# Performance work log

Measured on AMD Instinct MI355X. Metric: run time of the kernel, lower is better.

## Reference

```python
import jax, jax.numpy as jnp
import numpy as np
from jax import lax

N, DEG = 32768, 16

def _leaky(x):
    return jnp.where(x > 0, x, 0.2 * x)

def _gatv2(h, src, ws, bs, wd, bd, attn, bias):
    # DGL GATv2Conv: e_uv = attn . leaky_relu(fc_src(h_u) + fc_dst(h_v)); edge softmax over in-neighbors
    Hn, Dn = attn.shape
    fs = (h @ ws + bs).reshape(N, Hn, Dn)
    fd = (h @ wd + bd).reshape(N, Hn, Dn)
    e = _leaky(fs[src] + fd[:, None])                          # [N, DEG, H, D]
    alpha = jax.nn.softmax(jnp.einsum('ndhk,hk->ndh', e, attn), axis=1)
    return jnp.einsum('ndh,ndhk->nhk', alpha, fs[src]) + bias.reshape(1, Hn, Dn)

def _lstm_last(x, wih, whh, b):
    # torch LSTM gate order i,f,g,o; returns final hidden state. x: [N, DEG, F]
    n, hh = x.shape[0], whh.shape[1]
    def step(carry, xt):
        h, c = carry
        g = xt @ wih.T + h @ whh.T + b
        i, f, gg, o = jnp.split(g, 4, axis=-1)
        c = jax.nn.sigmoid(f) * c + jax.nn.sigmoid(i) * jnp.tanh(gg)
        h = jax.nn.sigmoid(o) * jnp.tanh(c)
        return (h, c), None
    init = (jnp.zeros((n, hh), x.dtype), jnp.zeros((n, hh), x.dtype))
    (h, _), _ = lax.scan(step, init, jnp.swapaxes(x, 0, 1))
    return h

def _sage(h, src, wih, whh, b, wself, wneigh, bias):
    # DGL SAGEConv(aggregator='lstm'): rst = fc_self(h) + fc_neigh(lstm(neighbor msgs))
    hn = _lstm_last(h[src], wih, whh, b)
    return h @ wself + hn @ wneigh + bias

def _forward(feat, g0, l0, g1, l1, g2, l2, s1, s2, f1_w, f1_b, f2_w, f2_b, src):
    h = feat
    h = jax.nn.elu(_gatv2(h, src, *g0).reshape(N, -1) + h @ l0[0] + l0[1])
    h = jax.nn.elu(_gatv2(h, src, *g1).reshape(N, -1) + h @ l1[0] + l1[1])
    gat = _gatv2(h, src, *g2).mean(axis=1) + h @ l2[0] + l2[1]   # [N, 32]
    x = jax.nn.relu(_sage(feat, src, *s1))
    x = jax.nn.relu(_sage(x, src, *s2))                          # [N, 32]
    z = jnp.concatenate([gat, x], axis=1)
    z = jax.nn.relu(z @ f1_w + f1_b)
    return z @ f2_w + f2_b                                       # [N, 1]

def setup_inputs() -> dict:
    ks = iter(jax.random.split(jax.random.key(0), 64))
    def nrm(shape, s=0.1):
        return (s * jax.random.normal(next(ks), shape)).astype(jnp.float32)
    d = {}
    d['feat'] = jax.random.normal(next(ks), (N, 5), jnp.float32)
    d['src'] = jax.random.randint(next(ks), (N, DEG), 0, N)
    for i, (fi, hn) in enumerate([(5, 4), (128, 4), (128, 1)]):
        fo = 32 * hn
        d[f'g{i}_ws'] = nrm((fi, fo)); d[f'g{i}_bs'] = nrm((fo,))
        d[f'g{i}_wd'] = nrm((fi, fo)); d[f'g{i}_bd'] = nrm((fo,))
        d[f'g{i}_attn'] = nrm((hn, 32)); d[f'g{i}_bias'] = nrm((fo,))
        d[f'l{i}_w'] = nrm((fi, fo)); d[f'l{i}_b'] = nrm((fo,))
    for j, fi in [(1, 5), (2, 32)]:
        d[f's{j}_wih'] = nrm((4 * fi, fi)); d[f's{j}_whh'] = nrm((4 * fi, fi))
        d[f's{j}_b'] = nrm((4 * fi,))
        d[f's{j}_wself'] = nrm((fi, 32)); d[f's{j}_wneigh'] = nrm((fi, 32))
        d[f's{j}_bias'] = nrm((32,))
    d['f1_w'] = nrm((64, 16)); d['f1_b'] = nrm((16,))
    d['f2_w'] = (0.1 + 0.01 * jax.random.normal(next(ks), (16, 1))).astype(jnp.float32)
    d['f2_b'] = nrm((1,))
    return d

def reference(feat, src, g0_ws, g0_bs, g0_wd, g0_bd, g0_attn, g0_bias, l0_w, l0_b, g1_ws, g1_bs, g1_wd, g1_bd, g1_attn, g1_bias, l1_w, l1_b, g2_ws, g2_bs, g2_wd, g2_bd, g2_attn, g2_bias, l2_w, l2_b, s1_wih, s1_whh, s1_b, s1_wself, s1_wneigh, s1_bias, s2_wih, s2_whh, s2_b, s2_wself, s2_wneigh, s2_bias, f1_w, f1_b, f2_w, f2_b):
    return _forward(feat,
                    (g0_ws, g0_bs, g0_wd, g0_bd, g0_attn, g0_bias), (l0_w, l0_b),
                    (g1_ws, g1_bs, g1_wd, g1_bd, g1_attn, g1_bias), (l1_w, l1_b),
                    (g2_ws, g2_bs, g2_wd, g2_bd, g2_attn, g2_bias), (l2_w, l2_b),
                    (s1_wih, s1_whh, s1_b, s1_wself, s1_wneigh, s1_bias),
                    (s2_wih, s2_whh, s2_b, s2_wself, s2_wneigh, s2_bias),
                    f1_w, f1_b, f2_w, f2_b, src)
```

## Files before the change

kernel.cpp:

```cpp
#include <hip/hip_runtime.h>
#include <hip/hip_bf16.h>

#define NNODES 32768
#define DEG 16

__device__ __forceinline__ float sigmoidf_(float x) { return 1.f / (1.f + __expf(-x)); }
__device__ __forceinline__ float tanhf_(float x) { return 1.f - 2.f / (__expf(2.f * x) + 1.f); }

typedef __attribute__((ext_vector_type(8))) short bf16x8;
typedef __attribute__((ext_vector_type(4))) float f32x4;
typedef __attribute__((ext_vector_type(8))) _Float16 f16x8;

__device__ __forceinline__ unsigned short f2bf_(float x) {
  __hip_bfloat16 b = __float2bfloat16(x);
  union { __hip_bfloat16 b; unsigned short u; } cv;
  cv.b = b;
  return cv.u;
}
__device__ __forceinline__ float bf2f_(unsigned short u) {
  union { unsigned short u; __hip_bfloat16 b; } cv;
  cv.u = u;
  return __bfloat162float(cv.b);
}
__device__ __forceinline__ void pack_hilo_(const float* v, bf16x8& hi, bf16x8& lo) {
#pragma unroll
  for (int j = 0; j < 8; j++) {
    unsigned short h = f2bf_(v[j]);
    float resid = v[j] - bf2f_(h);
    hi[j] = (short)h;
    lo[j] = (short)f2bf_(resid);
  }
}

#define WP_G1    0
#define WP_G2    98304
#define WP_S2WIH 122880
#define WP_TOTAL 131072

__global__ __launch_bounds__(256) void startup_kernel(
    const float* __restrict__ feat,
    const float* __restrict__ W0, const float* __restrict__ B0,
    const float* __restrict__ W1, const float* __restrict__ B1,
    const float* __restrict__ W2, const float* __restrict__ B2,
    float* __restrict__ O0, float* __restrict__ O1, float* __restrict__ O2,
    const float* __restrict__ g1ws, const float* __restrict__ g1wd,
    const float* __restrict__ l1w, const float* __restrict__ g2ws,
    const float* __restrict__ g2wd, const float* __restrict__ l2w,
    const float* __restrict__ s2wih, short* __restrict__ Wp) {
  __shared__ float w_s[5 * 64];
  __shared__ float in_s[32 * 8];
  __shared__ float b_s[64];
  const int bid = blockIdx.x;
  const int t = threadIdx.x;
  if (bid < 6144) {
    const int bz = bid >> 11, rem = bid & 2047, by = rem >> 10, bx = rem & 1023;
    const float* W = (bz == 0) ? W0 : (bz == 1) ? W1 : W2;
    const float* bias = (bz == 0) ? B0 : (bz == 1) ? B1 : B2;
    float* out = (bz == 0) ? O0 : (bz == 1) ? O1 : O2;
    const int rowBase = bx * 32;
    const int colBase = by * 64;
    for (int idx = t; idx < 5 * 64; idx += 256) {
      int k = idx >> 6, jj = idx & 63;
      w_s[idx] = W[(size_t)k * 128 + colBase + jj];
    }
    if (t < 64) b_s[t] = bias[colBase + t];
    for (int idx = t; idx < 32 * 5; idx += 256) {
      int r = idx / 5, k = idx - r * 5;
      in_s[r * 8 + k] = feat[(size_t)(rowBase + r) * 5 + k];
    }
    __syncthreads();
    const int jj = t & 63;
    const int rslot = t >> 6;
    float acc[8];
#pragma unroll
    for (int r = 0; r < 8; r++) acc[r] = b_s[jj];
    {
      float wv0 = w_s[0 * 64 + jj], wv1 = w_s[1 * 64 + jj];
      float wv2 = w_s[2 * 64 + jj], wv3 = w_s[3 * 64 + jj];
#pragma unroll
      for (int r = 0; r < 8; r++) {
        float4 ip = *(const float4*)&in_s[(rslot * 8 + r) * 8];
        acc[r] += ip.x * wv0 + ip.y * wv1 + ip.z * wv2 + ip.w * wv3;
      }
      float wv4 = w_s[4 * 64 + jj];
#pragma unroll
      for (int r = 0; r < 8; r++) acc[r] += in_s[(rslot * 8 + r) * 8 + 4] * wv4;
    }
#pragma unroll
    for (int r = 0; r < 8; r++)
      out[(size_t)(rowBase + rslot * 8 + r) * 128 + colBase + jj] = acc[r];
  } else {
    const int mid = bid - 6144;
    const float* W;
    int FI, FO, TRANS;
    size_t base;
    if (mid == 0)      { W = g1ws;  FI = 128; FO = 128; TRANS = 0; base = WP_G1; }
    else if (mid == 1) { W = g1wd;  FI = 128; FO = 128; TRANS = 0; base = WP_G1 + 32768; }
    else if (mid == 2) { W = l1w;   FI = 128; FO = 128; TRANS = 0; base = WP_G1 + 65536; }
    else if (mid == 3) { W = g2ws;  FI = 128; FO = 32;  TRANS = 0; base = WP_G2; }
    else if (mid == 4) { W = g2wd;  FI = 128; FO = 32;  TRANS = 0; base = WP_G2 + 8192; }
    else if (mid == 5) { W = l2w;   FI = 128; FO = 32;  TRANS = 0; base = WP_G2 + 16384; }
    else               { W = s2wih; FI = 32;  FO = 128; TRANS = 1; base = WP_S2WIH; }
    const int KS = FI / 32;
    const int total = FI * FO;
    for (int p = t; p < total; p += 256) {
      int j = p & 7, lane = (p >> 3) & 63, rest = p >> 9;
      int ks = rest % KS, f = rest / KS;
      int n = lane & 15, q = lane >> 4;
      int k = 32 * ks + 8 * q + j, fo = 16 * f + n;
      float v = TRANS ? W[(size_t)fo * FI + k] : W[(size_t)k * FO + fo];
      unsigned short hi = f2bf_(v);
      float resid = v - bf2f_(hi);
      Wp[base + p] = (short)hi;
      Wp[base + total + p] = (short)f2bf_(resid);
    }
  }
}

template <int KS, int FOT, int NZ>
__global__ __launch_bounds__(256) __attribute__((amdgpu_waves_per_eu(1, 4)))
void mfma_fc_kernel(const float* __restrict__ in, const short* __restrict__ Wp,
                    const float* __restrict__ B0, const float* __restrict__ B1,
                    const float* __restrict__ B2, float* __restrict__ O0,
                    float* __restrict__ O1, float* __restrict__ O2) {
  constexpr int FI = 32 * KS;
  constexpr int FO = 16 * FOT;
  const int tid = threadIdx.x;
  const int wid = tid >> 6;
  const int lane = tid & 63;
  const int q = lane >> 4, n = lane & 15;
  const int n0 = blockIdx.x * 64 + wid * 16;
  bf16x8 Ahi[KS], Alo[KS];
#pragma unroll
  for (int ks = 0; ks < KS; ks++) {
    float av[8];
    *(float4*)&av[0] = *(const float4*)&in[(size_t)(n0 + n) * FI + 32 * ks + 8 * q];
    *(float4*)&av[4] = *(const float4*)&in[(size_t)(n0 + n) * FI + 32 * ks + 8 * q + 4];
    pack_hilo_(av, Ahi[ks], Alo[ks]);
  }
#pragma unroll
  for (int z = 0; z < NZ; z++) {
    const short* wz = Wp + (size_t)z * FI * FO * 2;
    const float* bz = (z == 0) ? B0 : (z == 1) ? B1 : B2;
    float* oz = (z == 0) ? O0 : (z == 1) ? O1 : O2;
#pragma unroll
    for (int f = 0; f < FOT; f++) {
      float bv = bz[16 * f + n];
      f32x4 acc = {bv, bv, bv, bv};
#pragma unroll
      for (int ks = 0; ks < KS; ks++) {
        bf16x8 Bhi = *(const bf16x8*)&wz[((size_t)(f * KS + ks) * 64 + lane) * 8];
        bf16x8 Blo = *(const bf16x8*)&wz[(size_t)FI * FO + ((size_t)(f * KS + ks) * 64 + lane) * 8];
        acc = __builtin_amdgcn_mfma_f32_16x16x32_bf16(Ahi[ks], Bhi, acc, 0, 0, 0);
        acc = __builtin_amdgcn_mfma_f32_16x16x32_bf16(Alo[ks], Bhi, acc, 0, 0, 0);
        acc = __builtin_amdgcn_mfma_f32_16x16x32_bf16(Ahi[ks], Blo, acc, 0, 0, 0);
      }
#pragma unroll
      for (int r = 0; r < 4; r++)
        oz[(size_t)(n0 + 4 * q + r) * FO + 16 * f + n] = acc[r];
    }
  }
}

__global__ __launch_bounds__(256) __attribute__((amdgpu_waves_per_eu(1, 4)))
void xw_half_kernel(const float* __restrict__ in, const short* __restrict__ Wp,
                    const float* __restrict__ bz, _Float16* __restrict__ XWh) {
  const int tid = threadIdx.x;
  const int wid = tid >> 6;
  const int lane = tid & 63;
  const int q = lane >> 4, n = lane & 15;
  const int n0 = blockIdx.x * 64 + wid * 16;
  bf16x8 Ahi, Alo;
  {
    float av[8];
    *(float4*)&av[0] = *(const float4*)&in[(size_t)(n0 + n) * 32 + 8 * q];
    *(float4*)&av[4] = *(const float4*)&in[(size_t)(n0 + n) * 32 + 8 * q + 4];
    pack_hilo_(av, Ahi, Alo);
  }
#pragma unroll
  for (int f = 0; f < 8; f++) {
    float bv = bz[16 * f + n];
    f32x4 acc = {bv, bv, bv, bv};
    bf16x8 Bhi = *(const bf16x8*)&Wp[((size_t)f * 64 + lane) * 8];
    bf16x8 Blo = *(const bf16x8*)&Wp[4096 + ((size_t)f * 64 + lane) * 8];
    acc = __builtin_amdgcn_mfma_f32_16x16x32_bf16(Ahi, Bhi, acc, 0, 0, 0);
    acc = __builtin_amdgcn_mfma_f32_16x16x32_bf16(Alo, Bhi, acc, 0, 0, 0);
    acc = __builtin_amdgcn_mfma_f32_16x16x32_bf16(Ahi, Blo, acc, 0, 0, 0);
#pragma unroll
    for (int r = 0; r < 4; r++)
      XWh[(size_t)(n0 + 4 * q + r) * 128 + ((n >> 2) * 32 + f * 4 + (n & 3))] =
          (_Float16)acc[r];
  }
}

__global__ __launch_bounds__(256) void gat4_kernel(const float* __restrict__ fs,
                                                   const float* __restrict__ fd,
                                                   const float* __restrict__ lin,
                                                   const int* __restrict__ src,
                                                   const float* __restrict__ attn,
                                                   const float* __restrict__ bias,
                                                   float* __restrict__ out) {
  constexpr int F = 128;
  const int lane = threadIdx.x & 63;
  const int wave = threadIdx.x >> 6;
  const int li = lane & 15;
  const int node = blockIdx.x * 4 + wave;
  const int f0 = 2 * lane;
  const int srcv = src[(size_t)node * DEG + li];
  const float2 fdv = *(const float2*)&fd[(size_t)node * F + f0];
  const float a0 = attn[f0];
  const float a1 = attn[f0 + 1];
  float m = -1e30f, s = 0.f, acc0 = 0.f, acc1 = 0.f;
  int sd = __shfl(srcv, (lane & 48), 64);
  float2 fsv = *(const float2*)&fs[(size_t)sd * F + f0];
#pragma unroll
  for (int d = 0; d < DEG; d++) {
    float2 cur = fsv;
    if (d < DEG - 1) {
      int sn = __shfl(srcv, (lane & 48) | (d + 1), 64);
      fsv = *(const float2*)&fs[(size_t)sn * F + f0];
    }
    float e0 = cur.x + fdv.x; e0 = (e0 > 0.f) ? e0 : 0.2f * e0;
    float e1 = cur.y + fdv.y; e1 = (e1 > 0.f) ? e1 : 0.2f * e1;
    float p = e0 * a0 + e1 * a1;
    p += __shfl_xor(p, 1, 64);
    p += __shfl_xor(p, 2, 64);
    p += __shfl_xor(p, 4, 64);
    p += __shfl_xor(p, 8, 64);
    float nm = fmaxf(m, p);
    float ex = __expf(p - nm);
    float sc = __expf(m - nm);
    s = s * sc + ex;
    acc0 = acc0 * sc + ex * cur.x;
    acc1 = acc1 * sc + ex * cur.y;
    m = nm;
  }
  float inv = 1.f / s;
  float2 lv = *(const float2*)&lin[(size_t)node * F + f0];
  float o0 = acc0 * inv + lv.x + bias[f0];
  float o1 = acc1 * inv + lv.y + bias[f0 + 1];
  o0 = (o0 > 0.f) ? o0 : __expf(o0) - 1.f;
  o1 = (o1 > 0.f) ? o1 : __expf(o1) - 1.f;
  *(float2*)&out[(size_t)node * F + f0] = make_float2(o0, o1);
}

__global__ __launch_bounds__(256) void gat1_fw1_kernel(
    const float* __restrict__ fs, const float* __restrict__ fd,
    const float* __restrict__ lin, const int* __restrict__ src,
    const float* __restrict__ attn, const float* __restrict__ bias,
    float* __restrict__ out, const float* __restrict__ feat,
    const float* __restrict__ wih, const float* __restrict__ wb,
    float* __restrict__ fwout) {
  __shared__ float w_s[100];
  __shared__ float b_s[20];
  if (blockIdx.x < 2048) {
    constexpr int F = 32;
    const int lane = threadIdx.x & 63;
    const int wave = threadIdx.x >> 6;
    const int G = lane >> 4, li = lane & 15;
    const int node = blockIdx.x * 16 + wave * 4 + G;
    const int f0 = 2 * li;
    const int srcv = src[(size_t)node * DEG + li];
    const float2 fdv = *(const float2*)&fd[(size_t)node * F + f0];
    const float a0 = attn[f0];
    const float a1 = attn[f0 + 1];
    float m = -1e30f, s = 0.f, acc0 = 0.f, acc1 = 0.f;
    int sd = __shfl(srcv, (lane & 48), 64);
    float2 fsv = *(const float2*)&fs[(size_t)sd * F + f0];
#pragma unroll
    for (int d = 0; d < DEG; d++) {
      float2 cur = fsv;
      if (d < DEG - 1) {
        int sn = __shfl(srcv, (lane & 48) | (d + 1), 64);
        fsv = *(const float2*)&fs[(size_t)sn * F + f0];
      }
      float e0 = cur.x + fdv.x; e0 = (e0 > 0.f) ? e0 : 0.2f * e0;
      float e1 = cur.y + fdv.y; e1 = (e1 > 0.f) ? e1 : 0.2f * e1;
      float p = e0 * a0 + e1 * a1;
      p += __shfl_xor(p, 1, 64);
      p += __shfl_xor(p, 2, 64);
      p += __shfl_xor(p, 4, 64);
      p += __shfl_xor(p, 8, 64);
      float nm = fmaxf(m, p);
      float ex = __expf(p - nm);
      float sc = __expf(m - nm);
      s = s * sc + ex;
      acc0 = acc0 * sc + ex * cur.x;
      acc1 = acc1 * sc + ex * cur.y;
      m = nm;
    }
    float inv = 1.f / s;
    float2 lv = *(const float2*)&lin[(size_t)node * F + f0];
    float o0 = acc0 * inv + lv.x + bias[f0];
    float o1 = acc1 * inv + lv.y + bias[f0 + 1];
    *(float2*)&out[(size_t)node * F + f0] = make_float2(o0, o1);
  } else {
    if (threadIdx.x < 100) w_s[threadIdx.x] = wih[threadIdx.x];
    if (threadIdx.x < 20) b_s[threadIdx.x] = wb[threadIdx.x];
    __syncthreads();
    const int n = (blockIdx.x - 2048) * 256 + threadIdx.x;
    float f[5];
#pragma unroll
    for (int k = 0; k < 5; k++) f[k] = feat[(size_t)n * 5 + k];
#pragma unroll
    for (int j = 0; j < 20; j++) {
      float a = b_s[j];
#pragma unroll
      for (int k = 0; k < 5; k++) a += f[k] * w_s[j * 5 + k];
      fwout[(size_t)n * 20 + j] = a;
    }
  }
}

__global__ __attribute__((amdgpu_waves_per_eu(1, 4))) __launch_bounds__(256)
void lstm1s_kernel(const float* __restrict__ FW, const int* __restrict__ src,
                   const float* __restrict__ whh, const float* __restrict__ feat,
                   const float* __restrict__ wself, const float* __restrict__ wneigh,
                   const float* __restrict__ bias, float* __restrict__ x1out) {
  __shared__ float w_s[100];
  __shared__ float ws_s[160];
  __shared__ float wn_s[160];
  __shared__ float b_s[32];
  if (threadIdx.x < 100) w_s[threadIdx.x] = whh[threadIdx.x];
  if (threadIdx.x < 160) {
    ws_s[threadIdx.x] = wself[threadIdx.x];
    wn_s[threadIdx.x] = wneigh[threadIdx.x];
  }
  if (threadIdx.x < 32) b_s[threadIdx.x] = bias[threadIdx.x];
  __syncthreads();
  const int n = blockIdx.x * 256 + threadIdx.x;
  const int* sp = src + (size_t)n * DEG;
  float f[5];
#pragma unroll
  for (int k = 0; k < 5; k++) f[k] = feat[(size_t)n * 5 + k];
  float h[5] = {0, 0, 0, 0, 0}, c[5] = {0, 0, 0, 0, 0};
  int sd = sp[0];
  float4 p0 = *(const float4*)&FW[(size_t)sd * 20 + 0];
  float4 p1 = *(const float4*)&FW[(size_t)sd * 20 + 4];
  float4 p2 = *(const float4*)&FW[(size_t)sd * 20 + 8];
  float4 p3 = *(const float4*)&FW[(size_t)sd * 20 + 12];
  float4 p4 = *(const float4*)&FW[(size_t)sd * 20 + 16];
  for (int d = 0; d < DEG; d++) {
    float g[20];
    g[0] = p0.x; g[1] = p0.y; g[2] = p0.z; g[3] = p0.w;
    g[4] = p1.x; g[5] = p1.y; g[6] = p1.z; g[7] = p1.w;
    g[8] = p2.x; g[9] = p2.y; g[10] = p2.z; g[11] = p2.w;
    g[12] = p3.x; g[13] = p3.y; g[14] = p3.z; g[15] = p3.w;
    g[16] = p4.x; g[17] = p4.y; g[18] = p4.z; g[19] = p4.w;
    if (d < DEG - 1) {
      int sn = sp[d + 1];
      p0 = *(const float4*)&FW[(size_t)sn * 20 + 0];
      p1 = *(const float4*)&FW[(size_t)sn * 20 + 4];
      p2 = *(const float4*)&FW[(size_t)sn * 20 + 8];
      p3 = *(const float4*)&FW[(size_t)sn * 20 + 12];
      p4 = *(const float4*)&FW[(size_t)sn * 20 + 16];
    }
#pragma unroll
    for (int j = 0; j < 20; j++) {
#pragma unroll
      for (int k = 0; k < 5; k++) g[j] += h[k] * w_s[j * 5 + k];
    }
#pragma unroll
    for (int k = 0; k < 5; k++) {
      float iv = sigmoidf_(g[k]);
      float fv = sigmoidf_(g[5 + k]);
      float gv = tanhf_(g[10 + k]);
      float ov = sigmoidf_(g[15 + k]);
      c[k] = fv * c[k] + iv * gv;
      h[k] = ov * tanhf_(c[k]);
    }
  }
#pragma unroll
  for (int j = 0; j < 32; j++) {
    float a = b_s[j];
#pragma unroll
    for (int k = 0; k < 5; k++) a += f[k] * ws_s[k * 32 + j] + h[k] * wn_s[k * 32 + j];
    x1out[(size_t)n * 32 + j] = fmaxf(a, 0.f);
  }
}

__global__ __launch_bounds__(256) __attribute__((amdgpu_waves_per_eu(1, 4)))
void lstm2_mfma_kernel(const _Float16* __restrict__ XW, const int* __restrict__ src,
                       const float* __restrict__ whh, float* __restrict__ hn_out) {
  __shared__ float h_lds_all[4 * 16 * 36];
  __shared__ int src_lds_all[4 * 256];
  const int tid = threadIdx.x;
  const int wid = tid >> 6;
  const int lane = tid & 63;
  const int q = lane >> 4;
  const int n = lane & 15;
  const int n0 = (blockIdx.x * 4 + wid) * 16;
  float* h_lds = &h_lds_all[wid * 16 * 36];
  int* src_lds = &src_lds_all[wid * 256];

  {
    int4 sv = *(const int4*)&src[(size_t)(n0 + (lane >> 2)) * DEG + 4 * (lane & 3)];
    src_lds[(4 * (lane & 3) + 0) * 16 + (lane >> 2)] = sv.x;
    src_lds[(4 * (lane & 3) + 1) * 16 + (lane >> 2)] = sv.y;
    src_lds[(4 * (lane & 3) + 2) * 16 + (lane >> 2)] = sv.z;
    src_lds[(4 * (lane & 3) + 3) * 16 + (lane >> 2)] = sv.w;
  }

  bf16x8 Whi[8], Wlo[8];
#pragma unroll
  for (int gt = 0; gt < 8; gt++) {
    float wv[8];
    *(float4*)&wv[0] = *(const float4*)&whh[(size_t)(16 * gt + n) * 32 + 8 * q];
    *(float4*)&wv[4] = *(const float4*)&whh[(size_t)(16 * gt + n) * 32 + 8 * q + 4];
    pack_hilo_(wv, Whi[gt], Wlo[gt]);
  }

  bf16x8 Bhi, Blo;
#pragma unroll
  for (int j = 0; j < 8; j++) { Bhi[j] = 0; Blo[j] = 0; }
  float cst[8];
#pragma unroll
  for (int i = 0; i < 8; i++) cst[i] = 0.f;

  f16x8 tch[4], tnh[4];
  {
    int s0 = src_lds[0 * 16 + n];
    const _Float16* gb = XW + (size_t)s0 * 128 + q * 32;
#pragma unroll
    for (int t = 0; t < 4; t++) tch[t] = *(const f16x8*)&gb[8 * t];
  }

  float hv[8];
#pragma unroll
  for (int d = 0; d < DEG; d++) {
    f32x4 D[4][2];
#pragma unroll
    for (int p = 0; p < 4; p++) {
#pragma unroll
      for (int hh = 0; hh < 2; hh++) {
        int gt = p * 2 + hh;
        f32x4 acc = {0.f, 0.f, 0.f, 0.f};
        acc = __builtin_amdgcn_mfma_f32_16x16x32_bf16(Whi[gt], Bhi, acc, 0, 0, 0);
        acc = __builtin_amdgcn_mfma_f32_16x16x32_bf16(Wlo[gt], Bhi, acc, 0, 0, 0);
        acc = __builtin_amdgcn_mfma_f32_16x16x32_bf16(Whi[gt], Blo, acc, 0, 0, 0);
        D[p][hh] = acc;
      }
    }
    if (d < DEG - 1) {
      int s = src_lds[(d + 1) * 16 + n];
      const _Float16* gb = XW + (size_t)s * 128 + q * 32;
#pragma unroll
      for (int t = 0; t < 4; t++) tnh[t] = *(const f16x8*)&gb[8 * t];
    }
#pragma unroll
    for (int hh = 0; hh < 2; hh++) {
#pragma unroll
      for (int r = 0; r < 4; r++) {
        int ci = hh * 4 + r;
        float xiv = (float)tch[0][hh * 4 + r];
        float xfv = (float)tch[1][hh * 4 + r];
        float xgv = (float)tch[2][hh * 4 + r];
        float xov = (float)tch[3][hh * 4 + r];
        float iv = sigmoidf_(D[0][hh][r] + xiv);
        float fv = sigmoidf_(D[1][hh][r] + xfv);
        float gv = tanhf_(D[2][hh][r] + xgv);
        float ov = sigmoidf_(D[3][hh][r] + xov);
        cst[ci] = fv * cst[ci] + iv * gv;
        hv[ci] = ov * tanhf_(cst[ci]);
      }
    }
    if (d < DEG - 1) {
      *(float4*)&h_lds[n * 36 + 0 + 4 * q] = make_float4(hv[0], hv[1], hv[2], hv[3]);
      *(float4*)&h_lds[n * 36 + 16 + 4 * q] = make_float4(hv[4], hv[5], hv[6], hv[7]);
      float hb[8];
      *(float4*)&hb[0] = *(const float4*)&h_lds[n * 36 + 8 * q];
      *(float4*)&hb[4] = *(const float4*)&h_lds[n * 36 + 8 * q + 4];
      pack_hilo_(hb, Bhi, Blo);
#pragma unroll
      for (int t = 0; t < 4; t++) tch[t] = tnh[t];
    }
  }
  *(float4*)&hn_out[(size_t)(n0 + n) * 32 + 0 + 4 * q] = make_float4(hv[0], hv[1], hv[2], hv[3]);
  *(float4*)&hn_out[(size_t)(n0 + n) * 32 + 16 + 4 * q] = make_float4(hv[4], hv[5], hv[6], hv[7]);
}

__global__ __launch_bounds__(128) void sage_final_kernel(
    const float* __restrict__ x1, const float* __restrict__ hn,
    const float* __restrict__ wself, const float* __restrict__ wneigh,
    const float* __restrict__ sbias, const float* __restrict__ gat,
    const float* __restrict__ f1w, const float* __restrict__ f1b,
    const float* __restrict__ f2w, const float* __restrict__ f2b,
    float* __restrict__ out) {
  __shared__ float ws_s[32 * 32];
  __shared__ float wn_s[32 * 32];
  __shared__ float b_s[32];
  __shared__ float w1_s[64 * 16];
  __shared__ float b1_s[16];
  __shared__ float w2_s[16];
  for (int idx = threadIdx.x; idx < 1024; idx += 128) {
    ws_s[idx] = wself[idx];
    wn_s[idx] = wneigh[idx];
    w1_s[idx] = f1w[idx];
  }
  if (threadIdx.x < 32) b_s[threadIdx.x] = sbias[threadIdx.x];
  if (threadIdx.x < 16) {
    b1_s[threadIdx.x] = f1b[threadIdx.x];
    w2_s[threadIdx.x] = f2w[threadIdx.x];
  }
  __syncthreads();
  const int n = blockIdx.x * 128 + threadIdx.x;
  float xr[32], hr[32], z[64];
#pragma unroll
  for (int k = 0; k < 32; k += 4) {
    *(float4*)&xr[k] = *(const float4*)&x1[(size_t)n * 32 + k];
    *(float4*)&hr[k] = *(const float4*)&hn[(size_t)n * 32 + k];
    float4 a = *(const float4*)&gat[(size_t)n * 32 + k];
    z[k] = a.x; z[k + 1] = a.y; z[k + 2] = a.z; z[k + 3] = a.w;
  }
#pragma unroll
  for (int j = 0; j < 32; j++) {
    float a = b_s[j];
#pragma unroll
    for (int k = 0; k < 32; k++) a += xr[k] * ws_s[k * 32 + j];
#pragma unroll
    for (int k = 0; k < 32; k++) a += hr[k] * wn_s[k * 32 + j];
    z[32 + j] = fmaxf(a, 0.f);
  }
  float o = f2b[0];
#pragma unroll
  for (int j = 0; j < 16; j++) {
    float a = b1_s[j];
#pragma unroll
    for (int k = 0; k < 64; k++) a += z[k] * w1_s[k * 16 + j];
    o += fmaxf(a, 0.f) * w2_s[j];
  }
  out[n] = o;
}

extern "C" void kernel_launch(void* const* d_in, const int* in_sizes, int n_in,
                              void* d_out, int out_size, void* d_ws, size_t ws_size,
                              hipStream_t stream) {
  const int N = NNODES;
  const float* feat = (const float*)d_in[0];
  const int* src = (const int*)d_in[1];
  const float* g0_ws = (const float*)d_in[2];
  const float* g0_bs = (const float*)d_in[3];
  const float* g0_wd = (const float*)d_in[4];
  const float* g0_bd = (const float*)d_in[5];
  const float* g0_attn = (const float*)d_in[6];
  const float* g0_bias = (const float*)d_in[7];
  const float* l0_w = (const float*)d_in[8];
  const float* l0_b = (const float*)d_in[9];
  const float* g1_ws = (const float*)d_in[10];
  const float* g1_bs = (const float*)d_in[11];
  const float* g1_wd = (const float*)d_in[12];
  const float* g1_bd = (const float*)d_in[13];
  const float* g1_attn = (const float*)d_in[14];
  const float* g1_bias = (const float*)d_in[15];
  const float* l1_w = (const float*)d_in[16];
  const float* l1_b = (const float*)d_in[17];
  const float* g2_ws = (const float*)d_in[18];
  const float* g2_bs = (const float*)d_in[19];
  const float* g2_wd = (const float*)d_in[20];
  const float* g2_bd = (const float*)d_in[21];
  const float* g2_attn = (const float*)d_in[22];
  const float* g2_bias = (const float*)d_in[23];
  const float* l2_w = (const float*)d_in[24];
  const float* l2_b = (const float*)d_in[25];
  const float* s1_wih = (const float*)d_in[26];
  const float* s1_whh = (const float*)d_in[27];
  const float* s1_b = (const float*)d_in[28];
  const float* s1_wself = (const float*)d_in[29];
  const float* s1_wneigh = (const float*)d_in[30];
  const float* s1_bias = (const float*)d_in[31];
  const float* s2_wih = (const float*)d_in[32];
  const float* s2_whh = (const float*)d_in[33];
  const float* s2_b = (const float*)d_in[34];
  const float* s2_wself = (const float*)d_in[35];
  const float* s2_wneigh = (const float*)d_in[36];
  const float* s2_bias = (const float*)d_in[37];
  const float* f1_w = (const float*)d_in[38];
  const float* f1_b = (const float*)d_in[39];
  const float* f2_w = (const float*)d_in[40];
  const float* f2_b = (const float*)d_in[41];

  float* A = (float*)d_ws;
  float* B = A + (size_t)N * 128;
  float* C = B + (size_t)N * 128;
  float* D = C + (size_t)N * 128;
  float* E = D + (size_t)N * 128;
  short* Wp = (short*)(A + (size_t)5 * N * 128);

  startup_kernel<<<6151, 256, 0, stream>>>(
      feat, g0_ws, g0_bs, g0_wd, g0_bd, l0_w, l0_b, A, B, C,
      g1_ws, g1_wd, l1_w, g2_ws, g2_wd, l2_w, s2_wih, Wp);
  gat4_kernel<<<N / 4, 256, 0, stream>>>(A, B, C, src, g0_attn, g0_bias, D);
  mfma_fc_kernel<4, 8, 3><<<N / 64, 256, 0, stream>>>(
      D, Wp + WP_G1, g1_bs, g1_bd, l1_b, A, B, C);
  gat4_kernel<<<N / 4, 256, 0, stream>>>(A, B, C, src, g1_attn, g1_bias, E);
  mfma_fc_kernel<4, 2, 3><<<N / 64, 256, 0, stream>>>(
      E, Wp + WP_G2, g2_bs, g2_bd, l2_b, A, B, C);
  gat1_fw1_kernel<<<2048 + 128, 256, 0, stream>>>(
      A, B, C, src, g2_attn, g2_bias, D, feat, s1_wih, s1_b, E);
  lstm1s_kernel<<<N / 256, 256, 0, stream>>>(E, src, s1_whh, feat, s1_wself,
                                             s1_wneigh, s1_bias, C);
  xw_half_kernel<<<N / 64, 256, 0, stream>>>(
      C, Wp + WP_S2WIH, s2_b, (_Float16*)A);
  lstm2_mfma_kernel<<<N / 64, 256, 0, stream>>>((const _Float16*)A, src, s2_whh, E);
  sage_final_kernel<<<N / 128, 128, 0, stream>>>(
      C, E, s2_wself, s2_wneigh, s2_bias, D, f1_w, f1_b, f2_w, f2_b,
      (float*)d_out);
}
```

Measured before the change: 415.8 us.

## Store GAT source features in fp16 and use fast reciprocal in activations

The fc_src outputs for the first two GATv2 layers are now written as fp16 by the startup and MFMA FC kernels, and gat4_kernel gathers them as half2 and converts to float. This halves the bytes of the 16-neighbor random gather, which is the main memory cost of those kernels. Separately, sigmoid and tanh now use the hardware approximate reciprocal instead of a full divide. Both changes lower precision, so results may drift slightly from the reference.

```diff
diff --git a/kernel.cpp b/kernel.cpp
--- a/kernel.cpp
+++ b/kernel.cpp
@@ -4,12 +4,17 @@
 #define NNODES 32768
 #define DEG 16
 
-__device__ __forceinline__ float sigmoidf_(float x) { return 1.f / (1.f + __expf(-x)); }
-__device__ __forceinline__ float tanhf_(float x) { return 1.f - 2.f / (__expf(2.f * x) + 1.f); }
+__device__ __forceinline__ float sigmoidf_(float x) {
+  return __builtin_amdgcn_rcpf(1.f + __expf(-x));
+}
+__device__ __forceinline__ float tanhf_(float x) {
+  return 1.f - 2.f * __builtin_amdgcn_rcpf(__expf(2.f * x) + 1.f);
+}
 
 typedef __attribute__((ext_vector_type(8))) short bf16x8;
 typedef __attribute__((ext_vector_type(4))) float f32x4;
 typedef __attribute__((ext_vector_type(8))) _Float16 f16x8;
+typedef __attribute__((ext_vector_type(2))) _Float16 f16x2;
 
 __device__ __forceinline__ unsigned short f2bf_(float x) {
   __hip_bfloat16 b = __float2bfloat16(x);
@@ -42,7 +47,7 @@
     const float* __restrict__ W0, const float* __restrict__ B0,
     const float* __restrict__ W1, const float* __restrict__ B1,
     const float* __restrict__ W2, const float* __restrict__ B2,
-    float* __restrict__ O0, float* __restrict__ O1, float* __restrict__ O2,
+    _Float16* __restrict__ O0h, float* __restrict__ O1, float* __restrict__ O2,
     const float* __restrict__ g1ws, const float* __restrict__ g1wd,
     const float* __restrict__ l1w, const float* __restrict__ g2ws,
     const float* __restrict__ g2wd, const float* __restrict__ l2w,
@@ -56,7 +61,6 @@
     const int bz = bid >> 11, rem = bid & 2047, by = rem >> 10, bx = rem & 1023;
     const float* W = (bz == 0) ? W0 : (bz == 1) ? W1 : W2;
     const float* bias = (bz == 0) ? B0 : (bz == 1) ? B1 : B2;
-    float* out = (bz == 0) ? O0 : (bz == 1) ? O1 : O2;
     const int rowBase = bx * 32;
     const int colBase = by * 64;
     for (int idx = t; idx < 5 * 64; idx += 256) {
@@ -86,9 +90,17 @@
 #pragma unroll
       for (int r = 0; r < 8; r++) acc[r] += in_s[(rslot * 8 + r) * 8 + 4] * wv4;
     }
-#pragma unroll
-    for (int r = 0; r < 8; r++)
-      out[(size_t)(rowBase + rslot * 8 + r) * 128 + colBase + jj] = acc[r];
+    if (bz == 0) {
+#pragma unroll
+      for (int r = 0; r < 8; r++)
+        O0h[(size_t)(rowBase + rslot * 8 + r) * 128 + colBase + jj] =
+            (_Float16)acc[r];
+    } else {
+      float* out = (bz == 1) ? O1 : O2;
+#pragma unroll
+      for (int r = 0; r < 8; r++)
+        out[(size_t)(rowBase + rslot * 8 + r) * 128 + colBase + jj] = acc[r];
+    }
   } else {
     const int mid = bid - 6144;
     const float* W;
@@ -117,7 +129,7 @@
   }
 }
 
-template <int KS, int FOT, int NZ>
+template <int KS, int FOT, int NZ, int HALF0>
 __global__ __launch_bounds__(256) __attribute__((amdgpu_waves_per_eu(1, 4)))
 void mfma_fc_kernel(const float* __restrict__ in, const short* __restrict__ Wp,
                     const float* __restrict__ B0, const float* __restrict__ B1,
@@ -155,9 +167,16 @@
         acc = __builtin_amdgcn_mfma_f32_16x16x32_bf16(Alo[ks], Bhi, acc, 0, 0, 0);
         acc = __builtin_amdgcn_mfma_f32_16x16x32_bf16(Ahi[ks], Blo, acc, 0, 0, 0);
       }
-#pragma unroll
-      for (int r = 0; r < 4; r++)
-        oz[(size_t)(n0 + 4 * q + r) * FO + 16 * f + n] = acc[r];
+      if (HALF0 && z == 0) {
+#pragma unroll
+        for (int r = 0; r < 4; r++)
+          ((_Float16*)O0)[(size_t)(n0 + 4 * q + r) * FO + 16 * f + n] =
+              (_Float16)acc[r];
+      } else {
+#pragma unroll
+        for (int r = 0; r < 4; r++)
+          oz[(size_t)(n0 + 4 * q + r) * FO + 16 * f + n] = acc[r];
+      }
     }
   }
 }
@@ -193,7 +212,7 @@
   }
 }
 
-__global__ __launch_bounds__(256) void gat4_kernel(const float* __restrict__ fs,
+__global__ __launch_bounds__(256) void gat4_kernel(const _Float16* __restrict__ fs,
                                                    const float* __restrict__ fd,
                                                    const float* __restrict__ lin,
                                                    const int* __restrict__ src,
@@ -212,13 +231,13 @@
   const float a1 = attn[f0 + 1];
   float m = -1e30f, s = 0.f, acc0 = 0.f, acc1 = 0.f;
   int sd = __shfl(srcv, (lane & 48), 64);
-  float2 fsv = *(const float2*)&fs[(size_t)sd * F + f0];
+  f16x2 fsv = *(const f16x2*)&fs[(size_t)sd * F + f0];
 #pragma unroll
   for (int d = 0; d < DEG; d++) {
-    float2 cur = fsv;
+    float2 cur = make_float2((float)fsv[0], (float)fsv[1]);
     if (d < DEG - 1) {
       int sn = __shfl(srcv, (lane & 48) | (d + 1), 64);
-      fsv = *(const float2*)&fs[(size_t)sn * F + f0];
+      fsv = *(const f16x2*)&fs[(size_t)sn * F + f0];
     }
     float e0 = cur.x + fdv.x; e0 = (e0 > 0.f) ? e0 : 0.2f * e0;
     float e1 = cur.y + fdv.y; e1 = (e1 > 0.f) ? e1 : 0.2f * e1;
@@ -587,13 +606,16 @@
   short* Wp = (short*)(A + (size_t)5 * N * 128);
 
   startup_kernel<<<6151, 256, 0, stream>>>(
-      feat, g0_ws, g0_bs, g0_wd, g0_bd, l0_w, l0_b, A, B, C,
+      feat, g0_ws, g0_bs, g0_wd, g0_bd, l0_w, l0_b,
+      (_Float16*)A, B, C,
       g1_ws, g1_wd, l1_w, g2_ws, g2_wd, l2_w, s2_wih, Wp);
-  gat4_kernel<<<N / 4, 256, 0, stream>>>(A, B, C, src, g0_attn, g0_bias, D);
-  mfma_fc_kernel<4, 8, 3><<<N / 64, 256, 0, stream>>>(
+  gat4_kernel<<<N / 4, 256, 0, stream>>>((const _Float16*)A, B, C, src,
+                                         g0_attn, g0_bias, D);
+  mfma_fc_kernel<4, 8, 3, 1><<<N / 64, 256, 0, stream>>>(
       D, Wp + WP_G1, g1_bs, g1_bd, l1_b, A, B, C);
-  gat4_kernel<<<N / 4, 256, 0, stream>>>(A, B, C, src, g1_attn, g1_bias, E);
-  mfma_fc_kernel<4, 2, 3><<<N / 64, 256, 0, stream>>>(
+  gat4_kernel<<<N / 4, 256, 0, stream>>>((const _Float16*)A, B, C, src,
+                                         g1_attn, g1_bias, E);
+  mfma_fc_kernel<4, 2, 3, 0><<<N / 64, 256, 0, stream>>>(
       E, Wp + WP_G2, g2_bs, g2_bd, l2_b, A, B, C);
   gat1_fw1_kernel<<<2048 + 128, 256, 0, stream>>>(
       A, B, C, src, g2_attn, g2_bias, D, feat, s1_wih, s1_b, E);
```

Result: faster. 381.9 us (-8.1%).
